# Kernel tuning notes

Hardware: AMD Instinct MI355X
Metric: run time of the kernel (lower is better)

## Reference

```python
import jax, jax.numpy as jnp
import numpy as np

N_NODES = 50000
N_EDGES = 800000
NODE_DIM = 128
EDGE_DIM = 64
HID = 2 * NODE_DIM + EDGE_DIM  # 320


def setup_inputs() -> dict:
    key = jax.random.key(0)
    k1, k2, k3, k4 = jax.random.split(key, 4)
    x = jax.random.normal(k1, (N_NODES, NODE_DIM), dtype=jnp.float32)
    edge_index = jax.random.randint(k2, (2, N_EDGES), 0, N_NODES, dtype=jnp.int32)
    edge_ft = jax.random.normal(k3, (N_EDGES, EDGE_DIM), dtype=jnp.float32)
    kw1, kw2 = jax.random.split(k4)
    scale = 1.0 / np.sqrt(HID)
    W_val = jax.random.uniform(kw1, (NODE_DIM, HID), jnp.float32, -scale, scale)
    b_val = jnp.zeros((NODE_DIM,), jnp.float32)
    W_mul = jax.random.uniform(kw2, (NODE_DIM, HID), jnp.float32, -scale, scale)
    b_mul = jnp.zeros((NODE_DIM,), jnp.float32)
    return {"x": x, "edge_index": edge_index, "edge_ft": edge_ft,
            "W_val": W_val, "b_val": b_val, "W_mul": W_mul, "b_mul": b_mul}


def reference(x, edge_index, edge_ft, W_val, b_val, W_mul, b_mul):
    sender, receiver = edge_index[0], edge_index[1]
    # gather + concat: [E, 2*node_dim + edge_dim]
    c = jnp.concatenate([x[sender], x[receiver], edge_ft], axis=1)
    vals = jax.nn.softplus(c @ W_val.T + b_val)
    gate = jax.nn.sigmoid(c @ W_mul.T + b_mul)
    msg = vals * gate  # [E, node_dim]
    # scatter-sum by receiver into [N, node_dim]
    return jax.ops.segment_sum(msg, receiver, num_segments=x.shape[0])
```

## Files before the change

kernel.cpp:

```cpp
#include <hip/hip_runtime.h>

#define E_EDGES   800000
#define NN_NODES  50000
#define NODE_DIM  128
#define EDGE_DIM  64
#define KDIM      320
#define BM        64
#define BN        64
#define SWA       64
#define SM        132
#define SX        136
#define SO        264
#define SAF       72
#define THREADS   512
#define W4UNITS   20480
#define NSCAN     98

typedef _Float16 half8 __attribute__((ext_vector_type(8)));
typedef _Float16 half2t __attribute__((ext_vector_type(2)));
typedef __fp16   fp16x2 __attribute__((ext_vector_type(2)));
typedef float    f32x4 __attribute__((ext_vector_type(4)));

__device__ __forceinline__ unsigned short f2h(float f) {
    _Float16 h = (_Float16)f;
    return __builtin_bit_cast(unsigned short, h);
}
__device__ __forceinline__ float h2f(unsigned short u) {
    return (float)__builtin_bit_cast(_Float16, u);
}
__device__ __forceinline__ unsigned pkrtz(float a, float b) {
    fp16x2 r = __builtin_amdgcn_cvt_pkrtz(a, b);
    return __builtin_bit_cast(unsigned, r);
}

__global__ void prep(const float* __restrict__ wv,
                     const float* __restrict__ wm,
                     const int* __restrict__ ei,
                     unsigned short* __restrict__ Wc,
                     unsigned* __restrict__ cnt) {
    int i = blockIdx.x * blockDim.x + threadIdx.x;
    if (i < W4UNITS) {
        const int n4h = (NODE_DIM * KDIM) / 4;
        const float* src = (i < n4h) ? wv : wm;
        int j = (i < n4h) ? i : i - n4h;
        float4 f = ((const float4*)src)[j];
        uint2 o;
        o.x = pkrtz(f.x, f.y);
        o.y = pkrtz(f.z, f.w);
        ((uint2*)Wc)[i] = o;
    } else {
        int e = i - W4UNITS;
        if (e < E_EDGES) atomicAdd(&cnt[ei[E_EDGES + e]], 1u);
    }
}

__global__ void scan1(const unsigned* __restrict__ cnt,
                      unsigned* __restrict__ offs,
                      unsigned* __restrict__ bsum) {
    __shared__ unsigned s[512];
    int tid = threadIdx.x;
    int i = blockIdx.x * 512 + tid;
    unsigned v = (i < NN_NODES) ? cnt[i] : 0u;
    s[tid] = v; __syncthreads();
    for (int off = 1; off < 512; off <<= 1) {
        unsigned t = (tid >= off) ? s[tid - off] : 0u;
        __syncthreads();
        s[tid] += t;
        __syncthreads();
    }
    if (i < NN_NODES) offs[i] = s[tid] - v;
    if (tid == 511) bsum[blockIdx.x] = s[511];
}

__global__ void scan2(unsigned* __restrict__ bsum) {
    __shared__ unsigned s[128];
    int tid = threadIdx.x;
    unsigned v = (tid < NSCAN) ? bsum[tid] : 0u;
    s[tid] = v; __syncthreads();
    for (int off = 1; off < 128; off <<= 1) {
        unsigned t = (tid >= off) ? s[tid - off] : 0u;
        __syncthreads();
        s[tid] += t;
        __syncthreads();
    }
    if (tid < NSCAN) bsum[tid] = s[tid] - v;
}

__global__ void scatter_k(const int* __restrict__ ei,
                          unsigned* __restrict__ offs,
                          const unsigned* __restrict__ bsum,
                          unsigned* __restrict__ perm) {
    int e = blockIdx.x * blockDim.x + threadIdx.x;
    if (e >= E_EDGES) return;
    int r = ei[E_EDGES + e];
    unsigned p = atomicAdd(&offs[r], 1u) + bsum[r >> 9];
    perm[p] = (unsigned)e;
}

__global__ void __launch_bounds__(THREADS, 2)
pcompute(const float* __restrict__ x,
         const unsigned short* __restrict__ Wc,
         const float* __restrict__ bval,
         const float* __restrict__ bmul,
         unsigned short* __restrict__ Ph)
{
    __shared__ unsigned short Xs[BN * SX];
    __shared__ unsigned short Os[BN * SO];
    const int tid  = threadIdx.x;
    const int n0   = blockIdx.x * BN;
    const int lane = tid & 63;
    const int wid  = tid >> 6;
    const int wm   = wid & 1;
    const int wn   = wid >> 1;
    const int q    = lane >> 4;
    const int l16  = lane & 15;

#pragma unroll
    for (int i = 0; i < 2; ++i) {
        int u = tid + i * THREADS;
        int row = u >> 4, seg = u & 15;
        int node = n0 + row;
        if (node >= NN_NODES) node = NN_NODES - 1;
        const float* s = x + (size_t)node * NODE_DIM + seg * 8;
        float4 f0 = ((const float4*)s)[0];
        float4 f1 = ((const float4*)s)[1];
        uint4 v;
        v.x = pkrtz(f0.x, f0.y);
        v.y = pkrtz(f0.z, f0.w);
        v.z = pkrtz(f1.x, f1.y);
        v.w = pkrtz(f1.z, f1.w);
        *(uint4*)(&Xs[row * SX + seg * 8]) = v;
    }
    __syncthreads();

#pragma unroll
    for (int nhalf = 0; nhalf < 2; ++nhalf) {
        f32x4 acc[2][4];
        const f32x4 zero4 = {0.f, 0.f, 0.f, 0.f};
#pragma unroll
        for (int mt = 0; mt < 2; ++mt)
#pragma unroll
            for (int nt = 0; nt < 4; ++nt) acc[mt][nt] = zero4;

#pragma unroll
        for (int ks = 0; ks < 4; ++ks) {
            half8 a[2], b[4];
#pragma unroll
            for (int mt = 0; mt < 2; ++mt)
                a[mt] = *(const half8*)(&Xs[(wm * 32 + mt * 16 + l16) * SX + ks * 32 + q * 8]);
#pragma unroll
            for (int nt = 0; nt < 4; ++nt)
                b[nt] = *(const half8*)(Wc + (size_t)(wn * 64 + nt * 16 + l16) * KDIM
                                           + nhalf * 128 + ks * 32 + q * 8);
#pragma unroll
            for (int mt = 0; mt < 2; ++mt)
#pragma unroll
                for (int nt = 0; nt < 4; ++nt)
                    acc[mt][nt] = __builtin_amdgcn_mfma_f32_16x16x32_f16(
                        a[mt], b[nt], acc[mt][nt], 0, 0, 0);
        }

#pragma unroll
        for (int mt = 0; mt < 2; ++mt) {
#pragma unroll
            for (int nt = 0; nt < 4; ++nt) {
                int j  = wn * 64 + nt * 16 + l16;
                int c  = j & 127;
                int vg = j >> 7;
                float bb = 0.f;
                if (nhalf == 0) bb = vg ? bmul[c] : bval[c];
#pragma unroll
                for (int r = 0; r < 4; ++r) {
                    int row = wm * 32 + mt * 16 + q * 4 + r;
                    Os[row * SO + c * 2 + vg] = f2h(acc[mt][nt][r] + bb);
                }
            }
        }
        __syncthreads();

#pragma unroll
        for (int i = 0; i < 4; ++i) {
            int u = tid + i * THREADS;
            int row = u >> 5, seg = u & 31;
            int node = n0 + row;
            if (node < NN_NODES) {
                uint4 v = *(const uint4*)(&Os[row * SO + seg * 8]);
                *(uint4*)(Ph + (size_t)node * 512 + nhalf * 256 + seg * 8) = v;
            }
        }
        __syncthreads();
    }
}

__global__ void __launch_bounds__(THREADS, 4)
cgc_sorted(const unsigned short* __restrict__ Ph,
           const int* __restrict__ ei,
           const float* __restrict__ ef,
           const unsigned short* __restrict__ Wc,
           const unsigned* __restrict__ perm,
           float* __restrict__ out)
{
    __shared__ float msgBuf[BM * SM];
    __shared__ int  eIds[BM];
    __shared__ int  sIdx[BM];
    __shared__ int  rIdx[BM];
    __shared__ int  runStart[BM + 1];
    __shared__ int  slotRecv[BM];
    __shared__ int  nslotsS;

    unsigned short* As = (unsigned short*)msgBuf;

    const int tid  = threadIdx.x;
    const int e0   = blockIdx.x * BM;
    const int lane = tid & 63;
    const int wid  = tid >> 6;
    const int wm   = wid & 1;
    const int wn   = wid >> 1;
    const int q    = lane >> 4;
    const int l16  = lane & 15;

    if (tid < BM) {
        int e = (int)perm[e0 + tid];
        eIds[tid] = e;
        int sN = ei[e];
        int rN = ei[E_EDGES + e];
        sIdx[tid] = sN;
        rIdx[tid] = rN;
        int prev = __shfl_up(rN, 1);
        int flag = (tid == 0) || (prev != rN);
        unsigned long long m = __ballot(flag);
        int slot = __popcll(m & (((unsigned long long)2 << tid) - 1)) - 1;
        if (flag) { runStart[slot] = tid; slotRecv[slot] = rN; }
        if (tid == BM - 1) {
            int ns = (int)__popcll(m);
            nslotsS = ns;
            runStart[ns] = BM;
        }
    }
    __syncthreads();

    {
        int row = tid >> 3, seg = tid & 7;
        const float* s = ef + (size_t)eIds[row] * EDGE_DIM + seg * 8;
        float4 f0 = ((const float4*)s)[0];
        float4 f1 = ((const float4*)s)[1];
        uint4 v;
        v.x = pkrtz(f0.x, f0.y);
        v.y = pkrtz(f0.z, f0.w);
        v.z = pkrtz(f1.x, f1.y);
        v.w = pkrtz(f1.z, f1.w);
        int inner = (seg * 8) ^ ((row & 7) << 3);
        *(uint4*)(&As[row * SWA + inner]) = v;
    }

    const int nb0 = wn * 32;
    const int nbase[4] = { nb0, nb0 + 16, 128 + nb0, 128 + nb0 + 16 };
    half8 b[2][4];
#pragma unroll
    for (int ks = 0; ks < 2; ++ks)
#pragma unroll
        for (int nt = 0; nt < 4; ++nt)
            b[ks][nt] = *(const half8*)(Wc + (size_t)(nbase[nt] + l16) * KDIM
                                           + 256 + ks * 32 + q * 8);

    f32x4 acc[2][4];
    const f32x4 zero4 = {0.f, 0.f, 0.f, 0.f};
#pragma unroll
    for (int mt = 0; mt < 2; ++mt)
#pragma unroll
        for (int nt = 0; nt < 4; ++nt) acc[mt][nt] = zero4;

    __syncthreads();

#pragma unroll
    for (int ks = 0; ks < 2; ++ks) {
        half8 a[2];
#pragma unroll
        for (int mt = 0; mt < 2; ++mt) {
            int row = wm * 32 + mt * 16 + l16;
            int inner = (ks * 32 + q * 8) ^ ((row & 7) << 3);
            a[mt] = *(const half8*)(&As[row * SWA + inner]);
        }
#pragma unroll
        for (int mt = 0; mt < 2; ++mt)
#pragma unroll
            for (int nt = 0; nt < 4; ++nt)
                acc[mt][nt] = __builtin_amdgcn_mfma_f32_16x16x32_f16(
                    a[mt], b[ks][nt], acc[mt][nt], 0, 0, 0);
    }

    __syncthreads();

#pragma unroll
    for (int mt = 0; mt < 2; ++mt) {
#pragma unroll
        for (int r = 0; r < 4; ++r) {
            int row = wm * 32 + mt * 16 + q * 4 + r;
            int sN = sIdx[row];
            int rN = rIdx[row];
            const unsigned* pS = (const unsigned*)(Ph + ((size_t)sN << 9));
            const unsigned* pR = (const unsigned*)(Ph + ((size_t)rN << 9) + 256);
#pragma unroll
            for (int ct = 0; ct < 2; ++ct) {
                int c = wn * 32 + ct * 16 + l16;
                half2t hs = __builtin_bit_cast(half2t, pS[c]);
                half2t hr = __builtin_bit_cast(half2t, pR[c]);
                half2t t  = hs + hr;
                float v = acc[mt][ct][r]     + (float)t.x;
                float g = acc[mt][ct + 2][r] + (float)t.y;
                float sp  = fmaxf(v, 0.f) + __logf(1.f + __expf(-fabsf(v)));
                float sig = __builtin_amdgcn_rcpf(1.f + __expf(-g));
                msgBuf[row * SM + c] = sp * sig;
            }
        }
    }
    __syncthreads();

    const int nslots = nslotsS;
    for (int idx = tid; idx < nslots * NODE_DIM; idx += THREADS) {
        int s = idx >> 7, c = idx & 127;
        int rs = runStart[s], re = runStart[s + 1];
        float sum = 0.f;
        const float* p = &msgBuf[rs * SM + c];
        for (int row = rs; row < re; ++row) { sum += *p; p += SM; }
        atomicAdd(out + (size_t)slotRecv[s] * NODE_DIM + c, sum);
    }
}

__global__ void __launch_bounds__(THREADS, 4)
cgc_atomic(const unsigned short* __restrict__ Ph,
           const int* __restrict__ ei,
           const float* __restrict__ ef,
           const unsigned short* __restrict__ Wc,
           float* __restrict__ out)
{
    __shared__ unsigned short As[BM * SAF];
    __shared__ int sIdx[BM];
    __shared__ int rIdx[BM];

    const int tid  = threadIdx.x;
    const int e0   = blockIdx.x * BM;
    const int lane = tid & 63;
    const int wid  = tid >> 6;
    const int wm   = wid & 1;
    const int wn   = wid >> 1;
    const int q    = lane >> 4;
    const int l16  = lane & 15;

    if (tid < BM) {
        sIdx[tid] = ei[e0 + tid];
        rIdx[tid] = ei[E_EDGES + e0 + tid];
    }
    {
        int row = tid >> 3, seg = tid & 7;
        const float* s = ef + (size_t)(e0 + row) * EDGE_DIM + seg * 8;
        float4 f0 = ((const float4*)s)[0];
        float4 f1 = ((const float4*)s)[1];
        uint4 v;
        v.x = pkrtz(f0.x, f0.y);
        v.y = pkrtz(f0.z, f0.w);
        v.z = pkrtz(f1.x, f1.y);
        v.w = pkrtz(f1.z, f1.w);
        *(uint4*)(&As[row * SAF + seg * 8]) = v;
    }
    const int nb0 = wn * 32;
    const int nbase[4] = { nb0, nb0 + 16, 128 + nb0, 128 + nb0 + 16 };
    half8 b[2][4];
#pragma unroll
    for (int ks = 0; ks < 2; ++ks)
#pragma unroll
        for (int nt = 0; nt < 4; ++nt)
            b[ks][nt] = *(const half8*)(Wc + (size_t)(nbase[nt] + l16) * KDIM
                                           + 256 + ks * 32 + q * 8);
    f32x4 acc[2][4];
    const f32x4 zero4 = {0.f, 0.f, 0.f, 0.f};
#pragma unroll
    for (int mt = 0; mt < 2; ++mt)
#pragma unroll
        for (int nt = 0; nt < 4; ++nt) acc[mt][nt] = zero4;
    __syncthreads();
#pragma unroll
    for (int ks = 0; ks < 2; ++ks) {
        half8 a[2];
#pragma unroll
        for (int mt = 0; mt < 2; ++mt)
            a[mt] = *(const half8*)(&As[(wm * 32 + mt * 16 + l16) * SAF + ks * 32 + q * 8]);
#pragma unroll
        for (int mt = 0; mt < 2; ++mt)
#pragma unroll
            for (int nt = 0; nt < 4; ++nt)
                acc[mt][nt] = __builtin_amdgcn_mfma_f32_16x16x32_f16(
                    a[mt], b[ks][nt], acc[mt][nt], 0, 0, 0);
    }
#pragma unroll
    for (int mt = 0; mt < 2; ++mt) {
#pragma unroll
        for (int r = 0; r < 4; ++r) {
            int row = wm * 32 + mt * 16 + q * 4 + r;
            int sN = sIdx[row];
            int rN = rIdx[row];
            const unsigned* pS = (const unsigned*)(Ph + ((size_t)sN << 9));
            const unsigned* pR = (const unsigned*)(Ph + ((size_t)rN << 9) + 256);
#pragma unroll
            for (int ct = 0; ct < 2; ++ct) {
                int c = wn * 32 + ct * 16 + l16;
                half2t hs = __builtin_bit_cast(half2t, pS[c]);
                half2t hr = __builtin_bit_cast(half2t, pR[c]);
                half2t t  = hs + hr;
                float v = acc[mt][ct][r]     + (float)t.x;
                float g = acc[mt][ct + 2][r] + (float)t.y;
                float sp  = fmaxf(v, 0.f) + __logf(1.f + __expf(-fabsf(v)));
                float sig = __builtin_amdgcn_rcpf(1.f + __expf(-g));
                atomicAdd(out + (size_t)rN * NODE_DIM + c, sp * sig);
            }
        }
    }
}


extern "C" void kernel_launch(void* const* d_in, const int* in_sizes, int n_in,
                              void* d_out, int out_size, void* d_ws, size_t ws_size,
                              hipStream_t stream) {
    const float* x  = (const float*)d_in[0];
    const int*   ei = (const int*)d_in[1];
    const float* ef = (const float*)d_in[2];
    const float* Wv = (const float*)d_in[3];
    const float* bv = (const float*)d_in[4];
    const float* Wm = (const float*)d_in[5];
    const float* bm = (const float*)d_in[6];
    float* out = (float*)d_out;

    const size_t oWc   = 0;
    const size_t oPh   = 262144;
    const size_t oCnt  = oPh  + 51200000;
    const size_t oOffs = oCnt + 200704;
    const size_t oBsum = oOffs + 200704;
    const size_t oPerm = oBsum + 512;
    const size_t need_sorted = oPerm + (size_t)E_EDGES * 4;

    unsigned short* Wc = (unsigned short*)((char*)d_ws + oWc);
    unsigned short* Ph = (unsigned short*)((char*)d_ws + oPh);

    hipMemsetAsync(d_out, 0, (size_t)NN_NODES * NODE_DIM * sizeof(float), stream);

    if (ws_size >= need_sorted) {
        unsigned* cnt  = (unsigned*)((char*)d_ws + oCnt);
        unsigned* offs = (unsigned*)((char*)d_ws + oOffs);
        unsigned* bsum = (unsigned*)((char*)d_ws + oBsum);
        unsigned* perm = (unsigned*)((char*)d_ws + oPerm);

        hipMemsetAsync(cnt, 0, NN_NODES * sizeof(unsigned), stream);

        const int totalPrep = W4UNITS + E_EDGES;
        prep<<<(totalPrep + 255) / 256, 256, 0, stream>>>(Wv, Wm, ei, Wc, cnt);
        scan1<<<NSCAN, 512, 0, stream>>>(cnt, offs, bsum);
        scan2<<<1, 128, 0, stream>>>(bsum);
        scatter_k<<<(E_EDGES + 255) / 256, 256, 0, stream>>>(ei, offs, bsum, perm);

        pcompute<<<(NN_NODES + BN - 1) / BN, THREADS, 0, stream>>>(x, Wc, bv, bm, Ph);
        cgc_sorted<<<E_EDGES / BM, THREADS, 0, stream>>>(Ph, ei, ef, Wc, perm, out);
    } else {
        prep<<<(W4UNITS + 255) / 256, 256, 0, stream>>>(Wv, Wm, ei, Wc,
                                                        (unsigned*)((char*)d_ws + oPh));
        pcompute<<<(NN_NODES + BN - 1) / BN, THREADS, 0, stream>>>(x, Wc, bv, bm, Ph);
        cgc_atomic<<<E_EDGES / BM, THREADS, 0, stream>>>(Ph, ei, ef, Wc, out);
    }
}
```

Measured before the change: 563.2 us.

## Stage per-run receiver projections in LDS and store messages as fp16

Each block now preloads the receiver-side precomputed projection rows for up to 32 distinct receiver runs into shared memory. The epilogue then reads from LDS instead of issuing a global gather per edge row. To make room, the message buffer is stored as fp16 instead of fp32, which halves its LDS footprint but adds rounding before the per-run summation. Blocks with more than 32 runs fall back to global loads, and the extra staging pass adds a load phase before the MFMA loop.

New measurement: 592.9 us. 5.3% more time.

```diff
diff --git a/kernel.cpp b/kernel.cpp
--- a/kernel.cpp
+++ b/kernel.cpp
@@ -8,10 +8,11 @@
 #define BM        64
 #define BN        64
 #define SWA       64
-#define SM        132
+#define SMH       136
 #define SX        136
 #define SO        264
 #define SAF       72
+#define SLOTK     32
 #define THREADS   512
 #define W4UNITS   20480
 #define NSCAN     98
@@ -200,10 +201,11 @@
            const unsigned* __restrict__ perm,
            float* __restrict__ out)
 {
-    __shared__ float msgBuf[BM * SM];
+    __shared__ unsigned short msgBuf[BM * SMH];
+    __shared__ unsigned slotR[SLOTK * NODE_DIM];
     __shared__ int  eIds[BM];
     __shared__ int  sIdx[BM];
-    __shared__ int  rIdx[BM];
+    __shared__ int  slotOf[BM];
     __shared__ int  runStart[BM + 1];
     __shared__ int  slotRecv[BM];
     __shared__ int  nslotsS;
@@ -225,11 +227,11 @@
         int sN = ei[e];
         int rN = ei[E_EDGES + e];
         sIdx[tid] = sN;
-        rIdx[tid] = rN;
         int prev = __shfl_up(rN, 1);
         int flag = (tid == 0) || (prev != rN);
         unsigned long long m = __ballot(flag);
         int slot = __popcll(m & (((unsigned long long)2 << tid) - 1)) - 1;
+        slotOf[tid] = slot;
         if (flag) { runStart[slot] = tid; slotRecv[slot] = rN; }
         if (tid == BM - 1) {
             int ns = (int)__popcll(m);
@@ -253,6 +255,15 @@
         *(uint4*)(&As[row * SWA + inner]) = v;
     }
 
+    {
+        int ns = nslotsS < SLOTK ? nslotsS : SLOTK;
+        for (int u = tid; u < ns * 32; u += THREADS) {
+            int s = u >> 5, seg = u & 31;
+            uint4 v = ((const uint4*)(Ph + ((size_t)slotRecv[s] << 9) + 256))[seg];
+            *(uint4*)(&slotR[s * NODE_DIM + seg * 4]) = v;
+        }
+    }
+
     const int nb0 = wn * 32;
     const int nbase[4] = { nb0, nb0 + 16, 128 + nb0, 128 + nb0 + 16 };
     half8 b[2][4];
@@ -297,9 +308,11 @@
         for (int r = 0; r < 4; ++r) {
             int row = wm * 32 + mt * 16 + q * 4 + r;
             int sN = sIdx[row];
-            int rN = rIdx[row];
+            int slot = slotOf[row];
             const unsigned* pS = (const unsigned*)(Ph + ((size_t)sN << 9));
-            const unsigned* pR = (const unsigned*)(Ph + ((size_t)rN << 9) + 256);
+            const unsigned* pR = (slot < SLOTK)
+                ? &slotR[slot * NODE_DIM]
+                : (const unsigned*)(Ph + ((size_t)slotRecv[slot] << 9) + 256);
 #pragma unroll
             for (int ct = 0; ct < 2; ++ct) {
                 int c = wn * 32 + ct * 16 + l16;
@@ -310,7 +323,7 @@
                 float g = acc[mt][ct + 2][r] + (float)t.y;
                 float sp  = fmaxf(v, 0.f) + __logf(1.f + __expf(-fabsf(v)));
                 float sig = __builtin_amdgcn_rcpf(1.f + __expf(-g));
-                msgBuf[row * SM + c] = sp * sig;
+                msgBuf[row * SMH + c] = f2h(sp * sig);
             }
         }
     }
@@ -321,8 +334,8 @@
         int s = idx >> 7, c = idx & 127;
         int rs = runStart[s], re = runStart[s + 1];
         float sum = 0.f;
-        const float* p = &msgBuf[rs * SM + c];
-        for (int row = rs; row < re; ++row) { sum += *p; p += SM; }
+        const unsigned short* p = &msgBuf[rs * SMH + c];
+        for (int row = rs; row < re; ++row) { sum += h2f(*p); p += SMH; }
         atomicAdd(out + (size_t)slotRecv[s] * NODE_DIM + c, sum);
     }
 }
```

## Pack sorted edge tuples, batch Ph gathers, and store messages as fp16 in LDS

Applied to the files above, without the earlier changes.

The scatter step now writes a packed (edge, sender, receiver) record per sorted position, so the edge kernel no longer does dependent random reads of edge_index after reading perm. The Ph gathers for the epilogue are all issued up front into registers before any math, to give more memory-level parallelism. The message buffer in shared memory is stored as fp16 instead of fp32, which cuts LDS footprint and lets the segment reduction read two channels per load. The costs are a 16-byte-per-edge workspace array, more registers for the batched gathers, and lower precision for each message before it is summed.

After: 561.8 us. About the same (-0.2%).

```diff
diff --git a/kernel.cpp b/kernel.cpp
--- a/kernel.cpp
+++ b/kernel.cpp
@@ -8,7 +8,7 @@
 #define BM        64
 #define BN        64
 #define SWA       64
-#define SM        132
+#define SMH       136
 #define SX        136
 #define SO        264
 #define SAF       72
@@ -86,6 +86,18 @@
     if (tid < NSCAN) bsum[tid] = s[tid] - v;
 }
 
+__global__ void scatter_esr(const int* __restrict__ ei,
+                            unsigned* __restrict__ offs,
+                            const unsigned* __restrict__ bsum,
+                            uint4* __restrict__ esr) {
+    int e = blockIdx.x * blockDim.x + threadIdx.x;
+    if (e >= E_EDGES) return;
+    int s = ei[e];
+    int r = ei[E_EDGES + e];
+    unsigned p = atomicAdd(&offs[r], 1u) + bsum[r >> 9];
+    esr[p] = make_uint4((unsigned)e, (unsigned)s, (unsigned)r, 0u);
+}
+
 __global__ void scatter_k(const int* __restrict__ ei,
                           unsigned* __restrict__ offs,
                           const unsigned* __restrict__ bsum,
@@ -192,15 +204,17 @@
     }
 }
 
+template<bool USE_ESR>
 __global__ void __launch_bounds__(THREADS, 4)
 cgc_sorted(const unsigned short* __restrict__ Ph,
            const int* __restrict__ ei,
            const float* __restrict__ ef,
            const unsigned short* __restrict__ Wc,
            const unsigned* __restrict__ perm,
+           const uint4* __restrict__ esr,
            float* __restrict__ out)
 {
-    __shared__ float msgBuf[BM * SM];
+    __shared__ unsigned short msgBuf[BM * SMH];
     __shared__ int  eIds[BM];
     __shared__ int  sIdx[BM];
     __shared__ int  rIdx[BM];
@@ -220,10 +234,16 @@
     const int l16  = lane & 15;
 
     if (tid < BM) {
-        int e = (int)perm[e0 + tid];
+        int e, sN, rN;
+        if (USE_ESR) {
+            uint4 t = esr[e0 + tid];
+            e = (int)t.x; sN = (int)t.y; rN = (int)t.z;
+        } else {
+            e = (int)perm[e0 + tid];
+            sN = ei[e];
+            rN = ei[E_EDGES + e];
+        }
         eIds[tid] = e;
-        int sN = ei[e];
-        int rN = ei[E_EDGES + e];
         sIdx[tid] = sN;
         rIdx[tid] = rN;
         int prev = __shfl_up(rN, 1);
@@ -291,39 +311,58 @@
 
     __syncthreads();
 
+    unsigned usv[2][4][2], urv[2][4][2];
 #pragma unroll
     for (int mt = 0; mt < 2; ++mt) {
 #pragma unroll
         for (int r = 0; r < 4; ++r) {
             int row = wm * 32 + mt * 16 + q * 4 + r;
-            int sN = sIdx[row];
-            int rN = rIdx[row];
-            const unsigned* pS = (const unsigned*)(Ph + ((size_t)sN << 9));
-            const unsigned* pR = (const unsigned*)(Ph + ((size_t)rN << 9) + 256);
+            const unsigned* pS = (const unsigned*)(Ph + ((size_t)sIdx[row] << 9));
+            const unsigned* pR = (const unsigned*)(Ph + ((size_t)rIdx[row] << 9) + 256);
 #pragma unroll
             for (int ct = 0; ct < 2; ++ct) {
                 int c = wn * 32 + ct * 16 + l16;
-                half2t hs = __builtin_bit_cast(half2t, pS[c]);
-                half2t hr = __builtin_bit_cast(half2t, pR[c]);
+                usv[mt][r][ct] = pS[c];
+                urv[mt][r][ct] = pR[c];
+            }
+        }
+    }
+
+#pragma unroll
+    for (int mt = 0; mt < 2; ++mt) {
+#pragma unroll
+        for (int r = 0; r < 4; ++r) {
+            int row = wm * 32 + mt * 16 + q * 4 + r;
+#pragma unroll
+            for (int ct = 0; ct < 2; ++ct) {
+                int c = wn * 32 + ct * 16 + l16;
+                half2t hs = __builtin_bit_cast(half2t, usv[mt][r][ct]);
+                half2t hr = __builtin_bit_cast(half2t, urv[mt][r][ct]);
                 half2t t  = hs + hr;
                 float v = acc[mt][ct][r]     + (float)t.x;
                 float g = acc[mt][ct + 2][r] + (float)t.y;
                 float sp  = fmaxf(v, 0.f) + __logf(1.f + __expf(-fabsf(v)));
                 float sig = __builtin_amdgcn_rcpf(1.f + __expf(-g));
-                msgBuf[row * SM + c] = sp * sig;
+                msgBuf[row * SMH + c] = f2h(sp * sig);
             }
         }
     }
     __syncthreads();
 
     const int nslots = nslotsS;
-    for (int idx = tid; idx < nslots * NODE_DIM; idx += THREADS) {
-        int s = idx >> 7, c = idx & 127;
+    for (int idx = tid; idx < nslots * 64; idx += THREADS) {
+        int s = idx >> 6, cp = idx & 63;
         int rs = runStart[s], re = runStart[s + 1];
-        float sum = 0.f;
-        const float* p = &msgBuf[rs * SM + c];
-        for (int row = rs; row < re; ++row) { sum += *p; p += SM; }
-        atomicAdd(out + (size_t)slotRecv[s] * NODE_DIM + c, sum);
+        float s0 = 0.f, s1 = 0.f;
+        const unsigned* p = (const unsigned*)&msgBuf[rs * SMH + cp * 2];
+        for (int row = rs; row < re; ++row) {
+            half2t h = __builtin_bit_cast(half2t, *p);
+            s0 += (float)h.x; s1 += (float)h.y;
+            p += SMH / 2;
+        }
+        float* o = out + ((size_t)slotRecv[s] << 7) + cp * 2;
+        atomicAdd(o,     s0);
+        atomicAdd(o + 1, s1);
     }
 }
 
@@ -435,19 +474,19 @@
     const size_t oCnt  = oPh  + 51200000;
     const size_t oOffs = oCnt + 200704;
     const size_t oBsum = oOffs + 200704;
-    const size_t oPerm = oBsum + 512;
-    const size_t need_sorted = oPerm + (size_t)E_EDGES * 4;
+    const size_t oEsr  = oBsum + 512;
+    const size_t need_esr  = oEsr + (size_t)E_EDGES * 16;
+    const size_t need_perm = oEsr + (size_t)E_EDGES * 4;
 
     unsigned short* Wc = (unsigned short*)((char*)d_ws + oWc);
     unsigned short* Ph = (unsigned short*)((char*)d_ws + oPh);
 
     hipMemsetAsync(d_out, 0, (size_t)NN_NODES * NODE_DIM * sizeof(float), stream);
 
-    if (ws_size >= need_sorted) {
+    if (ws_size >= need_perm) {
         unsigned* cnt  = (unsigned*)((char*)d_ws + oCnt);
         unsigned* offs = (unsigned*)((char*)d_ws + oOffs);
         unsigned* bsum = (unsigned*)((char*)d_ws + oBsum);
-        unsigned* perm = (unsigned*)((char*)d_ws + oPerm);
 
         hipMemsetAsync(cnt, 0, NN_NODES * sizeof(unsigned), stream);
 
@@ -455,10 +494,20 @@
         prep<<<(totalPrep + 255) / 256, 256, 0, stream>>>(Wv, Wm, ei, Wc, cnt);
         scan1<<<NSCAN, 512, 0, stream>>>(cnt, offs, bsum);
         scan2<<<1, 128, 0, stream>>>(bsum);
-        scatter_k<<<(E_EDGES + 255) / 256, 256, 0, stream>>>(ei, offs, bsum, perm);
-
-        pcompute<<<(NN_NODES + BN - 1) / BN, THREADS, 0, stream>>>(x, Wc, bv, bm, Ph);
-        cgc_sorted<<<E_EDGES / BM, THREADS, 0, stream>>>(Ph, ei, ef, Wc, perm, out);
+
+        if (ws_size >= need_esr) {
+            uint4* esr = (uint4*)((char*)d_ws + oEsr);
+            scatter_esr<<<(E_EDGES + 255) / 256, 256, 0, stream>>>(ei, offs, bsum, esr);
+            pcompute<<<(NN_NODES + BN - 1) / BN, THREADS, 0, stream>>>(x, Wc, bv, bm, Ph);
+            cgc_sorted<true><<<E_EDGES / BM, THREADS, 0, stream>>>(
+                Ph, ei, ef, Wc, nullptr, esr, out);
+        } else {
+            unsigned* perm = (unsigned*)((char*)d_ws + oEsr);
+            scatter_k<<<(E_EDGES + 255) / 256, 256, 0, stream>>>(ei, offs, bsum, perm);
+            pcompute<<<(NN_NODES + BN - 1) / BN, THREADS, 0, stream>>>(x, Wc, bv, bm, Ph);
+            cgc_sorted<false><<<E_EDGES / BM, THREADS, 0, stream>>>(
+                Ph, ei, ef, Wc, perm, nullptr, out);
+        }
     } else {
         prep<<<(W4UNITS + 255) / 256, 256, 0, stream>>>(Wv, Wm, ei, Wc,
                                                         (unsigned*)((char*)d_ws + oPh));
```
